# Kernel tuning notes

Measured on AMD Instinct MI355X. Metric: run time of the kernel, lower is better.

Reference implementation:

```python
import jax, jax.numpy as jnp
import numpy as np

USER, ITEM, LATDIM, HYPER, FDIM, GL, LEAKY = 100000, 200000, 64, 128, 16, 2, 0.5
N = USER + ITEM
E = 3000000
LN_EPS = 1e-5


def _leaky(x):
    return jnp.where(x > 0, x, LEAKY * x)


def _ln(x, g, b):
    m = jnp.mean(x, axis=-1, keepdims=True)
    v = jnp.mean((x - m) ** 2, axis=-1, keepdims=True)
    return (x - m) * jax.lax.rsqrt(v + LN_EPS) * g + b


def _forward(fs, rows, cols):
    (uEmbeds, iEmbeds, uHyper, iHyper, u_attn, i_attn,
     dis_W1, dis_b1, dis_W2, dis_b2, dis_Wr1, dis_br1, dis_Wr2, dis_br2,
     dis_weights, dis_ln_g, dis_ln_b,
     gate_Wg1, gate_bg1, gate_Wg2, gate_bg2, gate_Wr1, gate_br1, gate_Wr2, gate_br2,
     gate_ln_g, gate_ln_b, adj_vals) = fs
    # Attention-weighted hyperedge incidence: softmax over the node axis (dim=0)
    uu = uEmbeds @ uHyper                       # [user, hyperNum]
    uu = uu * jax.nn.softmax(uu @ u_attn, axis=0)
    ii = iEmbeds @ iHyper                       # [item, hyperNum]
    ii = ii * jax.nn.softmax(ii @ i_attn, axis=0)
    x = jnp.concatenate([uEmbeds, iEmbeds], axis=0)  # [N, latdim]
    total = x
    for i in range(GL):
        # sparse GCN: spmm(adj, x) with COO edges (keepRate == 1 -> no edge drop)
        tem = jax.ops.segment_sum(adj_vals[:, None] * x[cols], rows, num_segments=N)
        # hypergraph conv: adj @ (adj.T @ x)
        hyp = jnp.concatenate([uu @ (uu.T @ x[:USER]), ii @ (ii.T @ x[USER:])], axis=0)

        def dis(z, j):
            # 4 disentanglers, batched over k via einsum
            h = _leaky(jnp.einsum('nd,kde->kne', z, dis_W1[i, j]) + dis_b1[i, j][:, None, :])
            f = jnp.einsum('kne,kef->knf', h, dis_W2[i, j]) + dis_b2[i, j][:, None, :]  # [4,N,fdim]
            comb = jnp.einsum('k,knf->nf', jax.nn.softmax(dis_weights[i, j]), f)
            rec = _leaky(comb @ dis_Wr1[i, j] + dis_br1[i, j]) @ dis_Wr2[i, j] + dis_br2[i, j]
            return _ln(z + rec, dis_ln_g[i, j], dis_ln_b[i, j])

        def gate(cur, prev):
            c = jnp.concatenate([cur, prev], axis=-1)  # [N, 2*latdim]
            gw = jax.nn.sigmoid(jax.nn.relu(c @ gate_Wg1[i] + gate_bg1[i]) @ gate_Wg2[i] + gate_bg2[i])
            res = _leaky(c @ gate_Wr1[i] + gate_br1[i]) @ gate_Wr2[i] + gate_br2[i]
            return _ln(gw * res + cur, gate_ln_g[i], gate_ln_b[i])

        x = gate(dis(tem, 0), x) + gate(dis(hyp, 1), x)
        total = total + x
    return total  # sum(lats): final node embeddings [N, latdim]


def setup_inputs() -> dict:
    key = jax.random.key(0)
    ks = iter(jax.random.split(key, 40))

    def rn(shape, scale=0.1):
        return jax.random.normal(next(ks), shape, dtype=jnp.float32) * scale

    return dict(
        uEmbeds=rn((USER, LATDIM)),
        iEmbeds=rn((ITEM, LATDIM)),
        uHyper=rn((LATDIM, HYPER)),
        iHyper=rn((LATDIM, HYPER)),
        u_attn=rn((HYPER, 1), 1.0),
        i_attn=rn((HYPER, 1), 1.0),
        dis_W1=rn((GL, 2, 4, LATDIM, LATDIM)),
        dis_b1=jnp.zeros((GL, 2, 4, LATDIM), jnp.float32),
        dis_W2=rn((GL, 2, 4, LATDIM, FDIM)),
        dis_b2=jnp.zeros((GL, 2, 4, FDIM), jnp.float32),
        dis_Wr1=rn((GL, 2, FDIM, LATDIM)),
        dis_br1=jnp.zeros((GL, 2, LATDIM), jnp.float32),
        dis_Wr2=rn((GL, 2, LATDIM, LATDIM)),
        dis_br2=jnp.zeros((GL, 2, LATDIM), jnp.float32),
        dis_weights=jnp.ones((GL, 2, 4), jnp.float32) / 4.0,
        dis_ln_g=jnp.ones((GL, 2, LATDIM), jnp.float32),
        dis_ln_b=jnp.zeros((GL, 2, LATDIM), jnp.float32),
        gate_Wg1=rn((GL, 2 * LATDIM, LATDIM)),
        gate_bg1=jnp.zeros((GL, LATDIM), jnp.float32),
        gate_Wg2=rn((GL, LATDIM, LATDIM)),
        gate_bg2=jnp.zeros((GL, LATDIM), jnp.float32),
        gate_Wr1=rn((GL, 2 * LATDIM, LATDIM)),
        gate_br1=jnp.zeros((GL, LATDIM), jnp.float32),
        gate_Wr2=rn((GL, LATDIM, LATDIM)),
        gate_br2=jnp.zeros((GL, LATDIM), jnp.float32),
        gate_ln_g=jnp.ones((GL, LATDIM), jnp.float32),
        gate_ln_b=jnp.zeros((GL, LATDIM), jnp.float32),
        adj_vals=jax.random.uniform(next(ks), (E,), dtype=jnp.float32) * 0.1,
        adj_rows=jax.random.randint(next(ks), (E,), 0, N, dtype=jnp.int32),
        adj_cols=jax.random.randint(next(ks), (E,), 0, N, dtype=jnp.int32),
        keep_rate=1,
    )


def reference(uEmbeds, iEmbeds, uHyper, iHyper, u_attn, i_attn,
              dis_W1, dis_b1, dis_W2, dis_b2, dis_Wr1, dis_br1, dis_Wr2, dis_br2,
              dis_weights, dis_ln_g, dis_ln_b,
              gate_Wg1, gate_bg1, gate_Wg2, gate_bg2, gate_Wr1, gate_br1, gate_Wr2, gate_br2,
              gate_ln_g, gate_ln_b, adj_vals, adj_rows, adj_cols, keep_rate):
    fs = (uEmbeds, iEmbeds, uHyper, iHyper, u_attn, i_attn,
          dis_W1, dis_b1, dis_W2, dis_b2, dis_Wr1, dis_br1, dis_Wr2, dis_br2,
          dis_weights, dis_ln_g, dis_ln_b,
          gate_Wg1, gate_bg1, gate_Wg2, gate_bg2, gate_Wr1, gate_br1, gate_Wr2, gate_br2,
          gate_ln_g, gate_ln_b, adj_vals)
    return _forward(fs, adj_rows, adj_cols)
```

## Files before the change

kernel.cpp:

```cpp
#include <hip/hip_runtime.h>
#include <math.h>

#define USERN 100000
#define ITEMN 200000
#define NND   300000
#define DD    64
#define HH    128
#define FF    16
#define EDG   3000000
#define LEAKY_A 0.5f
#define LN_EPS  1e-5f
#define SCHUNK 1024
#define SNB ((NND+SCHUNK-1)/SCHUNK)
#define PROWS (NND/8)
#define VQ 81910.0f

typedef __attribute__((ext_vector_type(8))) short bf16x8;
typedef __attribute__((ext_vector_type(4))) float f32x4;
#define MFMA16(a,b,c) __builtin_amdgcn_mfma_f32_16x16x32_bf16(a,b,c,0,0,0)
#define NTL(p) __builtin_nontemporal_load(p)

__device__ __forceinline__ float leaky(float x){ return x>0.f ? x : LEAKY_A*x; }
__device__ __forceinline__ unsigned fenc(float f){ unsigned u=__float_as_uint(f); return (u&0x80000000u)? ~u : (u|0x80000000u); }
__device__ __forceinline__ float fdec(unsigned u){ return (u&0x80000000u)? __uint_as_float(u&0x7fffffffu) : __uint_as_float(~u); }
__device__ __forceinline__ short f2bf(float f){
  unsigned u=__float_as_uint(f);
  unsigned r=u + 0x7fffu + ((u>>16)&1u);
  return (short)(r>>16);
}
__device__ __forceinline__ unsigned f2bf2(float lo, float hi){
  unsigned r;
  asm("v_cvt_pk_bf16_f32 %0, %1, %2" : "=v"(r) : "v"(lo), "v"(hi));
  return r;
}
__device__ __forceinline__ float bf2f(short s){
  return __uint_as_float(((unsigned)(unsigned short)s)<<16);
}
__device__ __forceinline__ bf16x8 loadAbf(const short* __restrict__ base, int l, int dbase){
  const short* p = base + (size_t)(l&15)*DD + dbase + ((l>>4)<<2);
  int2 a=*(const int2*)p;
  int2 b=*(const int2*)(p+16);
  bf16x8 r;
  ((int2*)&r)[0]=a; ((int2*)&r)[1]=b;
  return r;
}

__global__ __launch_bounds__(256) void k_init(const float* __restrict__ uE, const float* __restrict__ iE,
                        short* __restrict__ x){
  int tot=NND*DD;
  for(int idx=blockIdx.x*256+threadIdx.x; idx<tot; idx+=gridDim.x*256){
    float v=(idx<USERN*DD)? uE[idx] : iE[idx-USERN*DD];
    x[idx]=f2bf(v);
  }
}

__global__ __launch_bounds__(128) void k_hv(const float* __restrict__ uH,const float* __restrict__ iH,
      const float* __restrict__ uA,const float* __restrict__ iA,float* __restrict__ hv){
  int t=threadIdx.x;
  const float* H=(t<64)? uH:iH;
  const float* A=(t<64)? uA:iA;
  int d=t&63;
  float s=0.f;
  for(int h=0;h<HH;h++) s=fmaf(H[d*HH+h],A[h],s);
  hv[t]=s;
}

__global__ __launch_bounds__(256) void k_att(const float* __restrict__ E, const float* __restrict__ hvp,
      float* __restrict__ a, int U){
  __shared__ float hs[64];
  int tid=threadIdx.x;
  if(tid<64) hs[tid]=hvp[tid];
  __syncthreads();
  int wave=tid>>6, lane=tid&63;
  for(int g=blockIdx.x*4+wave; g<U/4; g+=gridDim.x*4){
    int n0=g*4;
    #pragma unroll
    for(int m=0;m<4;m++){
      float p=E[(size_t)(n0+m)*DD+lane]*hs[lane];
      #pragma unroll
      for(int off=32;off;off>>=1) p+=__shfl_xor(p,off,64);
      if(lane==0) a[n0+m]=p;
    }
  }
}

__global__ __launch_bounds__(256) void k_redmax(const float* __restrict__ a, int n, unsigned* slot){
  float v=-3.0e38f;
  for(int i=blockIdx.x*256+threadIdx.x;i<n;i+=gridDim.x*256) v=fmaxf(v,a[i]);
  #pragma unroll
  for(int off=32;off;off>>=1) v=fmaxf(v,__shfl_xor(v,off,64));
  if((threadIdx.x&63)==0) atomicMax(slot, fenc(v));
}

__global__ __launch_bounds__(256) void k_sumexp(const float* __restrict__ a, int n,
      const unsigned* __restrict__ mslot, float* ssum){
  float mx=fdec(*mslot);
  float s=0.f;
  for(int i=blockIdx.x*256+threadIdx.x;i<n;i+=gridDim.x*256) s+=expf(a[i]-mx);
  #pragma unroll
  for(int off=32;off;off>>=1) s+=__shfl_xor(s,off,64);
  if((threadIdx.x&63)==0) atomicAdd(ssum, s);
}

__global__ __launch_bounds__(256) void k_scale_a(float* __restrict__ a,int n,
      const unsigned* __restrict__ mslot,const float* __restrict__ ssum){
  float mx=fdec(*mslot); float inv=1.f/(*ssum);
  for(int i=blockIdx.x*256+threadIdx.x;i<n;i+=gridDim.x*256) a[i]=expf(a[i]-mx)*inv;
}

__global__ __launch_bounds__(256) void k_hist8(const int* __restrict__ rows, int* __restrict__ cnt){
  int part=blockIdx.x&7;
  int bip=blockIdx.x>>3, nbp=gridDim.x>>3;
  int lo=part*PROWS, hi=lo+PROWS;
  for(int e=bip*256+threadIdx.x; e<EDG; e+=nbp*256){
    int r=NTL(rows+e);
    if(r>=lo && r<hi) atomicAdd(&cnt[r],1);
  }
}

__global__ __launch_bounds__(256) void k_scanA(int* __restrict__ cnt, int* __restrict__ bsum){
  __shared__ int part[256];
  int b=blockIdx.x, t=threadIdx.x;
  int base=b*SCHUNK;
  int v[4]; int s=0;
  #pragma unroll
  for(int k2=0;k2<4;k2++){
    int idx=base+t*4+k2;
    int val=(idx<NND)? cnt[idx]:0;
    v[k2]=s; s+=val;
  }
  part[t]=s;
  __syncthreads();
  for(int off=1;off<256;off<<=1){
    int y=(t>=off)? part[t-off]:0;
    __syncthreads();
    part[t]+=y;
    __syncthreads();
  }
  int excl=(t==0)?0:part[t-1];
  #pragma unroll
  for(int k2=0;k2<4;k2++){
    int idx=base+t*4+k2;
    if(idx<NND) cnt[idx]=excl+v[k2];
  }
  if(t==255) bsum[b]=part[255];
}

__global__ __launch_bounds__(512) void k_scanB(int* __restrict__ bsum){
  __shared__ int part[512];
  int t=threadIdx.x;
  part[t]=(t<SNB)? bsum[t]:0;
  __syncthreads();
  for(int off=1;off<512;off<<=1){
    int y=(t>=off)? part[t-off]:0;
    __syncthreads();
    part[t]+=y;
    __syncthreads();
  }
  if(t<SNB) bsum[t]=(t==0)?0:part[t-1];
}

__global__ __launch_bounds__(256) void k_scanC(int* __restrict__ rowptr, const int* __restrict__ bsum,
      int* __restrict__ wcur){
  for(int i=blockIdx.x*256+threadIdx.x; i<NND; i+=gridDim.x*256){
    int v=rowptr[i]+bsum[i>>10];
    rowptr[i]=v; wcur[i]=v;
  }
  if(blockIdx.x==0 && threadIdx.x==0) rowptr[NND]=EDG;
}

__global__ __launch_bounds__(256) void k_scatter8(const int* __restrict__ rows,const int* __restrict__ cols,
      const float* __restrict__ vals, int* __restrict__ wcur, unsigned* __restrict__ epack){
  int part=blockIdx.x&7;
  int bip=blockIdx.x>>3, nbp=gridDim.x>>3;
  int lo=part*PROWS, hi=lo+PROWS;
  for(int e=bip*256+threadIdx.x; e<EDG; e+=nbp*256){
    int r=NTL(rows+e);
    if(r>=lo && r<hi){
      int pos=atomicAdd(&wcur[r],1);
      unsigned q=(unsigned)(NTL(vals+e)*VQ + 0.5f);
      epack[pos]=((unsigned)NTL(cols+e)<<13) | (q & 8191u);
    }
  }
}

__global__ __launch_bounds__(512) void k_spmm_csr(const int* __restrict__ rowptr,
      const unsigned* __restrict__ epack,
      const short* __restrict__ x, short* __restrict__ tem){
  int wave=threadIdx.x>>6, q4=(threadIdx.x>>4)&3, ln=threadIdx.x&15;
  const float dq=1.0f/VQ;
  for(int r=blockIdx.x*32+wave*4+q4; r<NND; r+=gridDim.x*32){
    int st=rowptr[r], en=rowptr[r+1];
    float a0=0.f,a1=0.f,a2=0.f,a3=0.f;
    int p=st;
    for(; p+1<en; p+=2){
      unsigned w0=NTL(epack+p), w1=NTL(epack+p+1);
      int c0=w0>>13, c1=w1>>13;
      float v0=(float)(w0&8191u)*dq, v1=(float)(w1&8191u)*dq;
      int2 x0=*(const int2*)(x+(size_t)c0*DD+ln*4);
      int2 x1=*(const int2*)(x+(size_t)c1*DD+ln*4);
      a0=fmaf(v0, bf2f((short)(x0.x&0xffff)), a0);
      a1=fmaf(v0, bf2f((short)(x0.x>>16)),    a1);
      a2=fmaf(v0, bf2f((short)(x0.y&0xffff)), a2);
      a3=fmaf(v0, bf2f((short)(x0.y>>16)),    a3);
      a0=fmaf(v1, bf2f((short)(x1.x&0xffff)), a0);
      a1=fmaf(v1, bf2f((short)(x1.x>>16)),    a1);
      a2=fmaf(v1, bf2f((short)(x1.y&0xffff)), a2);
      a3=fmaf(v1, bf2f((short)(x1.y>>16)),    a3);
    }
    if(p<en){
      unsigned w0=NTL(epack+p);
      int c0=w0>>13;
      float v0=(float)(w0&8191u)*dq;
      int2 x0=*(const int2*)(x+(size_t)c0*DD+ln*4);
      a0=fmaf(v0, bf2f((short)(x0.x&0xffff)), a0);
      a1=fmaf(v0, bf2f((short)(x0.x>>16)),    a1);
      a2=fmaf(v0, bf2f((short)(x0.y&0xffff)), a2);
      a3=fmaf(v0, bf2f((short)(x0.y>>16)),    a3);
    }
    int2 outw;
    outw.x=(int)f2bf2(a0,a1);
    outw.y=(int)f2bf2(a2,a3);
    *(int2*)(tem+(size_t)r*DD+ln*4) = outw;
  }
}

__global__ __launch_bounds__(256) void k_gacc(const float* __restrict__ E,const float* __restrict__ sca,
      const short* __restrict__ x,float* __restrict__ G,int U){
  __shared__ __align__(16) float es[4][256];
  int tid=threadIdx.x, wave=tid>>6, lane=tid&63;
  float acc[64];
  #pragma unroll
  for(int j=0;j<64;j++) acc[j]=0.f;
  float* esw=es[wave];
  for(int g=blockIdx.x*4+wave; g<U/4; g+=gridDim.x*4){
    int n0=g*4;
    float xv[4];
    #pragma unroll
    for(int m=0;m<4;m++){
      float sc=sca[n0+m];
      esw[m*64+lane]=E[(size_t)(n0+m)*DD+lane]*sc;
      xv[m]=bf2f(x[(size_t)(n0+m)*DD+lane]);
    }
    #pragma unroll
    for(int d4=0;d4<16;d4++){
      float4 eb[4];
      #pragma unroll
      for(int m=0;m<4;m++) eb[m]=((const float4*)(esw+m*64))[d4];
      #pragma unroll
      for(int c=0;c<4;c++){
        #pragma unroll
        for(int m=0;m<4;m++) acc[d4*4+c]=fmaf(((const float*)&eb[m])[c],xv[m],acc[d4*4+c]);
      }
    }
  }
  #pragma unroll
  for(int j=0;j<64;j++) atomicAdd(&G[j*64+lane],acc[j]);
}

__global__ __launch_bounds__(256) void k_tm(const float* __restrict__ uH,const float* __restrict__ iH,
      const float* __restrict__ G,float* __restrict__ Mo){
  __shared__ __align__(16) float Hs[64*HH];
  __shared__ __align__(16) float Gs[64*64];
  __shared__ __align__(16) float Ts[HH*64];
  const float* H = blockIdx.x ? iH : uH;
  const float* Gp = G + blockIdx.x*4096;
  float* Mp = Mo + blockIdx.x*4096;
  int tid=threadIdx.x;
  for(int k=tid;k<64*HH;k+=256) Hs[k]=H[k];
  for(int k=tid;k<4096;k+=256) Gs[k]=Gp[k];
  __syncthreads();
  int lane=tid&63, wq=tid>>6;
  float tac[32];
  #pragma unroll
  for(int k=0;k<32;k++) tac[k]=0.f;
  for(int d1=0;d1<64;d1++){
    float gv=Gs[d1*64+lane];
    const float4* hrow=(const float4*)(Hs+d1*HH+wq*32);
    #pragma unroll
    for(int k4=0;k4<8;k4++){
      float4 hb=hrow[k4];
      tac[k4*4+0]=fmaf(hb.x,gv,tac[k4*4+0]);
      tac[k4*4+1]=fmaf(hb.y,gv,tac[k4*4+1]);
      tac[k4*4+2]=fmaf(hb.z,gv,tac[k4*4+2]);
      tac[k4*4+3]=fmaf(hb.w,gv,tac[k4*4+3]);
    }
  }
  #pragma unroll
  for(int k=0;k<32;k++) Ts[(wq*32+k)*64+lane]=tac[k];
  __syncthreads();
  float mac[16];
  #pragma unroll
  for(int k=0;k<16;k++) mac[k]=0.f;
  for(int h=0;h<HH;h++){
    float tv=Ts[h*64+lane];
    #pragma unroll
    for(int k=0;k<16;k++) mac[k]=fmaf(Hs[(wq*16+k)*HH+h],tv,mac[k]);
  }
  #pragma unroll
  for(int k=0;k<16;k++) Mp[(wq*16+k)*64+lane]=mac[k];
}

__global__ __launch_bounds__(256) void k_hyp2(const float* __restrict__ E,const float* __restrict__ sca,
      const float* __restrict__ Mp,short* __restrict__ hyp,int U){
  __shared__ __align__(16) float es[4][256];
  int tid=threadIdx.x, wave=tid>>6, lane=tid&63;
  float mcol[64];
  #pragma unroll
  for(int j=0;j<64;j++) mcol[j]=Mp[j*64+lane];
  float* esw=es[wave];
  for(int g=blockIdx.x*4+wave; g<U/4; g+=gridDim.x*4){
    int n0=g*4;
    #pragma unroll
    for(int m=0;m<4;m++){
      float sc=sca[n0+m];
      esw[m*64+lane]=E[(size_t)(n0+m)*DD+lane]*sc;
    }
    float acc[4]={0,0,0,0};
    #pragma unroll
    for(int d4=0;d4<16;d4++){
      float4 eb[4];
      #pragma unroll
      for(int m=0;m<4;m++) eb[m]=((const float4*)(esw+m*64))[d4];
      #pragma unroll
      for(int c=0;c<4;c++){
        float mv=mcol[d4*4+c];
        #pragma unroll
        for(int m=0;m<4;m++) acc[m]=fmaf(((const float*)&eb[m])[c],mv,acc[m]);
      }
    }
    unsigned p01=f2bf2(acc[0],acc[1]), p23=f2bf2(acc[2],acc[3]);
    hyp[(size_t)(n0+0)*DD+lane]=(short)p01;
    hyp[(size_t)(n0+1)*DD+lane]=(short)(p01>>16);
    hyp[(size_t)(n0+2)*DD+lane]=(short)p23;
    hyp[(size_t)(n0+3)*DD+lane]=(short)(p23>>16);
  }
}

__global__ __launch_bounds__(512) void k_dis2(
    short* __restrict__ tem, short* __restrict__ hyp,
    const float* __restrict__ W1b,const float* __restrict__ b1b,
    const float* __restrict__ W2b,const float* __restrict__ b2b,
    const float* __restrict__ Wr1b,const float* __restrict__ br1b,
    const float* __restrict__ Wr2b,const float* __restrict__ br2b,
    const float* __restrict__ wsoftb,const float* __restrict__ lngb,const float* __restrict__ lnbb,
    int layer){
  __shared__ __align__(16) short w1s[16384];
  __shared__ __align__(16) short w2s[4096];
  __shared__ __align__(16) short wr1s[2048];
  __shared__ __align__(16) short wr2s[4096];
  __shared__ __align__(16) short hst[8][1024];
  __shared__ __align__(16) short cst[8][512];
  __shared__ float swsh[4];
  int half=gridDim.x>>1;
  int sel=(blockIdx.x>=half);
  int bid=blockIdx.x - (sel? half:0);
  int ij=layer*2+sel;
  short* z = sel? hyp : tem;
  const float* W1 = W1b + (size_t)ij*4*64*64;
  const float* b1 = b1b + (size_t)ij*4*64;
  const float* W2 = W2b + (size_t)ij*4*64*16;
  const float* b2 = b2b + (size_t)ij*4*16;
  const float* Wr1= Wr1b+ (size_t)ij*16*64;
  const float* br1= br1b+ (size_t)ij*64;
  const float* Wr2= Wr2b+ (size_t)ij*64*64;
  const float* br2= br2b+ (size_t)ij*64;
  const float* wsoft=wsoftb+(size_t)ij*4;
  const float* lng= lngb + (size_t)ij*64;
  const float* lnb= lnbb + (size_t)ij*64;
  int tid=threadIdx.x;
  for(int t=tid;t<16384;t+=512){
    int j=t&7,kg=(t>>3)&3,c=(t>>5)&15,ot=(t>>9)&3,kb=(t>>11)&1,kk=t>>12;
    int k=kb*32+kg*4+(j&3)+((j>>2)<<4), o=ot*16+c;
    w1s[t]=f2bf(W1[(size_t)(kk*64+k)*64+o]);
  }
  for(int t=tid;t<4096;t+=512){
    int j=t&7,kg=(t>>3)&3,c=(t>>5)&15,kb=(t>>9)&1,kk=t>>10;
    int k=kb*32+kg*4+(j&3)+((j>>2)<<4);
    w2s[t]=f2bf(W2[(size_t)(kk*64+k)*16+c]);
  }
  for(int t=tid;t<2048;t+=512){
    int j=t&7,kg=(t>>3)&3,c=(t>>5)&15,ot=t>>9;
    int o=ot*16+c;
    short v=0;
    if(j<4){ int k=kg*4+j; v=f2bf(Wr1[k*64+o]); }
    wr1s[t]=v;
  }
  for(int t=tid;t<4096;t+=512){
    int j=t&7,kg=(t>>3)&3,c=(t>>5)&15,ot=(t>>9)&3,kb=t>>11;
    int k=kb*32+kg*4+(j&3)+((j>>2)<<4), o=ot*16+c;
    wr2s[t]=f2bf(Wr2[k*64+o]);
  }
  if(tid==0){
    float m0=fmaxf(fmaxf(wsoft[0],wsoft[1]),fmaxf(wsoft[2],wsoft[3]));
    float e0=expf(wsoft[0]-m0),e1=expf(wsoft[1]-m0),e2=expf(wsoft[2]-m0),e3=expf(wsoft[3]-m0);
    float s=e0+e1+e2+e3;
    swsh[0]=e0/s; swsh[1]=e1/s; swsh[2]=e2/s; swsh[3]=e3/s;
  }
  __syncthreads();
  int wave=tid>>6, l=tid&63, lr=l&15, lg=l>>4;
  float sw[4]; sw[0]=swsh[0]; sw[1]=swsh[1]; sw[2]=swsh[2]; sw[3]=swsh[3];
  float b1v[4][4], br1v[4], br2v[4], gv[4], bv[4];
  #pragma unroll
  for(int kk=0;kk<4;kk++)
    #pragma unroll
    for(int ot=0;ot<4;ot++) b1v[kk][ot]=b1[kk*64+ot*16+lr];
  float b2c = sw[0]*b2[lr] + sw[1]*b2[16+lr] + sw[2]*b2[32+lr] + sw[3]*b2[48+lr];
  #pragma unroll
  for(int ot=0;ot<4;ot++){
    br1v[ot]=br1[ot*16+lr]; br2v[ot]=br2[ot*16+lr];
    gv[ot]=lng[ot*16+lr];   bv[ot]=lnb[ot*16+lr];
  }
  short* hw=hst[wave];
  short* cw=cst[wave];
  for(int t=l;t<256;t+=64){
    int r=t>>4, lgp=(t>>2)&3, jj=t&3;
    cw[(r*4+lgp)*8+4+jj]=0;
  }
  int slot=(lr*4+lg)*8;
  int sbase=((lg*4)*4 + (lr>>2))*8 + (l&3);
  const f32x4 zero={0.f,0.f,0.f,0.f};
  for(int tile=bid*8+wave; tile<NND/16; tile+=half*8){
    int n0=tile*16;
    short* zrow=z+(size_t)n0*DD;
    bf16x8 A0=loadAbf(zrow,l,0), A1=loadAbf(zrow,l,32);
    f32x4 cba; cba[0]=b2c; cba[1]=b2c; cba[2]=b2c; cba[3]=b2c;
    #pragma unroll
    for(int kk=0;kk<4;kk++){
      const short* w1k=&w1s[kk*4096];
      #pragma unroll
      for(int ot=0;ot<4;ot++){
        f32x4 ha=zero;
        ha=MFMA16(A0,*(const bf16x8*)&w1k[ot*512+slot],ha);
        ha=MFMA16(A1,*(const bf16x8*)&w1k[2048+ot*512+slot],ha);
        float bb=b1v[kk][ot];
        unsigned p01=f2bf2(leaky(ha[0]+bb), leaky(ha[1]+bb));
        unsigned p23=f2bf2(leaky(ha[2]+bb), leaky(ha[3]+bb));
        int base=(ot>>1)*512 + sbase + ((ot&1)<<2);
        hw[base   ]=(short)p01;
        hw[base+32]=(short)(p01>>16);
        hw[base+64]=(short)p23;
        hw[base+96]=(short)(p23>>16);
      }
      bf16x8 hA0=*(const bf16x8*)&hw[slot];
      bf16x8 hA1=*(const bf16x8*)&hw[512+slot];
      f32x4 fa=zero;
      fa=MFMA16(hA0,*(const bf16x8*)&w2s[kk*1024+slot],fa);
      fa=MFMA16(hA1,*(const bf16x8*)&w2s[kk*1024+512+slot],fa);
      float swk=sw[kk];
      #pragma unroll
      for(int j=0;j<4;j++) cba[j]=fmaf(swk,fa[j],cba[j]);
    }
    {
      int cbase=((lg*4)*4 + (lr>>2))*8 + (lr&3);
      unsigned c01=f2bf2(cba[0],cba[1]), c23=f2bf2(cba[2],cba[3]);
      cw[cbase   ]=(short)c01;
      cw[cbase+32]=(short)(c01>>16);
      cw[cbase+64]=(short)c23;
      cw[cbase+96]=(short)(c23>>16);
    }
    bf16x8 cA=*(const bf16x8*)&cw[slot];
    #pragma unroll
    for(int ot=0;ot<4;ot++){
      f32x4 ra=MFMA16(cA,*(const bf16x8*)&wr1s[ot*512+slot],zero);
      float bb=br1v[ot];
      unsigned p01=f2bf2(leaky(ra[0]+bb), leaky(ra[1]+bb));
      unsigned p23=f2bf2(leaky(ra[2]+bb), leaky(ra[3]+bb));
      int base=(ot>>1)*512 + sbase + ((ot&1)<<2);
      hw[base   ]=(short)p01;
      hw[base+32]=(short)(p01>>16);
      hw[base+64]=(short)p23;
      hw[base+96]=(short)(p23>>16);
    }
    bf16x8 rA0=*(const bf16x8*)&hw[slot];
    bf16x8 rA1=*(const bf16x8*)&hw[512+slot];
    float y[4][4];
    #pragma unroll
    for(int ot=0;ot<4;ot++){
      f32x4 rc=zero;
      rc=MFMA16(rA0,*(const bf16x8*)&wr2s[ot*512+slot],rc);
      rc=MFMA16(rA1,*(const bf16x8*)&wr2s[2048+ot*512+slot],rc);
      #pragma unroll
      for(int j=0;j<4;j++){
        float zd=bf2f(zrow[(size_t)(lg*4+j)*DD + ot*16+lr]);
        y[ot][j]=zd + rc[j] + br2v[ot];
      }
    }
    #pragma unroll
    for(int j=0;j<4;j++){
      float s=y[0][j]+y[1][j]+y[2][j]+y[3][j];
      s+=__shfl_xor(s,1,64); s+=__shfl_xor(s,2,64); s+=__shfl_xor(s,4,64); s+=__shfl_xor(s,8,64);
      float mean=s*(1.f/64.f);
      float t0=y[0][j]-mean, t1=y[1][j]-mean, t2=y[2][j]-mean, t3=y[3][j]-mean;
      float s2=t0*t0+t1*t1+t2*t2+t3*t3;
      s2+=__shfl_xor(s2,1,64); s2+=__shfl_xor(s2,2,64); s2+=__shfl_xor(s2,4,64); s2+=__shfl_xor(s2,8,64);
      float inv=rsqrtf(s2*(1.f/64.f)+LN_EPS);
      unsigned q01=f2bf2(t0*inv*gv[0]+bv[0], t1*inv*gv[1]+bv[1]);
      unsigned q23=f2bf2(t2*inv*gv[2]+bv[2], t3*inv*gv[3]+bv[3]);
      size_t row=(size_t)(lg*4+j)*DD;
      zrow[row +  0+lr]=(short)q01;
      zrow[row + 16+lr]=(short)(q01>>16);
      zrow[row + 32+lr]=(short)q23;
      zrow[row + 48+lr]=(short)(q23>>16);
    }
  }
}

__global__ __launch_bounds__(512) void k_gate2(
    const short* __restrict__ tem, const short* __restrict__ hyp,
    const short* __restrict__ xin, short* __restrict__ xout,
    const float* __restrict__ uEo, const float* __restrict__ iEo, float* __restrict__ outp, int doOut,
    const float* __restrict__ Wg1,const float* __restrict__ bg1,
    const float* __restrict__ Wg2,const float* __restrict__ bg2,
    const float* __restrict__ Wr1,const float* __restrict__ br1,
    const float* __restrict__ Wr2,const float* __restrict__ br2,
    const float* __restrict__ lng,const float* __restrict__ lnb){
  __shared__ __align__(16) short g1s[4*4*512];
  __shared__ __align__(16) short r1s[4*4*512];
  __shared__ __align__(16) short g2s[2*4*512];
  __shared__ __align__(16) short r2s[2*4*512];
  __shared__ __align__(16) short hls[8][2][1024];
  int tid=threadIdx.x;
  for(int t=tid;t<8192;t+=512){
    int j=t&7,kg=(t>>3)&3,c=(t>>5)&15,ot=(t>>9)&3,kb=t>>11;
    int k=kb*32+kg*4+(j&3)+((j>>2)<<4), o=ot*16+c;
    g1s[t]=f2bf(Wg1[k*64+o]);
    r1s[t]=f2bf(Wr1[k*64+o]);
  }
  for(int t=tid;t<4096;t+=512){
    int j=t&7,kg=(t>>3)&3,c=(t>>5)&15,ot=(t>>9)&3,kb=t>>11;
    int k=kb*32+kg*4+(j&3)+((j>>2)<<4), o=ot*16+c;
    g2s[t]=f2bf(Wg2[k*64+o]);
    r2s[t]=f2bf(Wr2[k*64+o]);
  }
  __syncthreads();
  int wave=tid>>6, l=tid&63;
  int lr=l&15, lg=l>>4;
  float bg1v[4],br1v[4],bg2v[4],br2v[4],gv[4],bv[4];
  #pragma unroll
  for(int ot=0;ot<4;ot++){
    bg1v[ot]=bg1[ot*16+lr]; br1v[ot]=br1[ot*16+lr];
    bg2v[ot]=bg2[ot*16+lr]; br2v[ot]=br2[ot*16+lr];
    gv[ot]=lng[ot*16+lr];   bv[ot]=lnb[ot*16+lr];
  }
  short* hG=&hls[wave][0][0];
  short* hR=&hls[wave][1][0];
  int slot=(lr*4+lg)*8;
  int sbase=((lg*4)*4 + (lr>>2))*8 + (l&3);
  const f32x4 zero={0.f,0.f,0.f,0.f};
  for(int tile=blockIdx.x*8+wave; tile<NND/16; tile+=gridDim.x*8){
    int n0=tile*16;
    const short* xrow=xin+(size_t)n0*DD;
    bf16x8 pA0=loadAbf(xrow,l,0), pA1=loadAbf(xrow,l,32);
    f32x4 pg[4],pr[4];
    #pragma unroll
    for(int ot=0;ot<4;ot++){
      f32x4 ag=zero, ar=zero;
      ag=MFMA16(pA0,*(const bf16x8*)&g1s[(2*4+ot)*512+slot],ag);
      ag=MFMA16(pA1,*(const bf16x8*)&g1s[(3*4+ot)*512+slot],ag);
      ar=MFMA16(pA0,*(const bf16x8*)&r1s[(2*4+ot)*512+slot],ar);
      ar=MFMA16(pA1,*(const bf16x8*)&r1s[(3*4+ot)*512+slot],ar);
      pg[ot]=ag; pr[ot]=ar;
    }
    float ya[4][4];
    #pragma unroll
    for(int p=0;p<2;p++){
      const short* cur=(p? hyp : tem)+(size_t)n0*DD;
      bf16x8 cA0=loadAbf(cur,l,0), cA1=loadAbf(cur,l,32);
      #pragma unroll
      for(int ot=0;ot<4;ot++){
        f32x4 ag=pg[ot], ar=pr[ot];
        ag=MFMA16(cA0,*(const bf16x8*)&g1s[(0*4+ot)*512+slot],ag);
        ag=MFMA16(cA1,*(const bf16x8*)&g1s[(1*4+ot)*512+slot],ag);
        ar=MFMA16(cA0,*(const bf16x8*)&r1s[(0*4+ot)*512+slot],ar);
        ar=MFMA16(cA1,*(const bf16x8*)&r1s[(1*4+ot)*512+slot],ar);
        float bgv=bg1v[ot], brv=br1v[ot];
        unsigned g01=f2bf2(fmaxf(ag[0]+bgv,0.f), fmaxf(ag[1]+bgv,0.f));
        unsigned g23=f2bf2(fmaxf(ag[2]+bgv,0.f), fmaxf(ag[3]+bgv,0.f));
        unsigned r01=f2bf2(leaky(ar[0]+brv), leaky(ar[1]+brv));
        unsigned r23=f2bf2(leaky(ar[2]+brv), leaky(ar[3]+brv));
        int base=(ot>>1)*512 + sbase + ((ot&1)<<2);
        hG[base   ]=(short)g01;  hG[base+32]=(short)(g01>>16);
        hG[base+64]=(short)g23;  hG[base+96]=(short)(g23>>16);
        hR[base   ]=(short)r01;  hR[base+32]=(short)(r01>>16);
        hR[base+64]=(short)r23;  hR[base+96]=(short)(r23>>16);
      }
      bf16x8 hgA0=*(const bf16x8*)&hG[slot],    hgA1=*(const bf16x8*)&hG[512+slot];
      bf16x8 hrA0=*(const bf16x8*)&hR[slot],    hrA1=*(const bf16x8*)&hR[512+slot];
      f32x4 g2a[4], r2a[4];
      #pragma unroll
      for(int ot=0;ot<4;ot++){
        f32x4 ag=zero, ar=zero;
        ag=MFMA16(hgA0,*(const bf16x8*)&g2s[(0*4+ot)*512+slot],ag);
        ag=MFMA16(hgA1,*(const bf16x8*)&g2s[(1*4+ot)*512+slot],ag);
        ar=MFMA16(hrA0,*(const bf16x8*)&r2s[(0*4+ot)*512+slot],ar);
        ar=MFMA16(hrA1,*(const bf16x8*)&r2s[(1*4+ot)*512+slot],ar);
        g2a[ot]=ag; r2a[ot]=ar;
      }
      float y[4][4];
      #pragma unroll
      for(int ot=0;ot<4;ot++){
        #pragma unroll
        for(int j=0;j<4;j++){
          float cd=bf2f(cur[(size_t)(lg*4+j)*DD + ot*16+lr]);
          float gw=1.f/(1.f+expf(-(g2a[ot][j]+bg2v[ot])));
          y[ot][j]=gw*(r2a[ot][j]+br2v[ot])+cd;
        }
      }
      #pragma unroll
      for(int j=0;j<4;j++){
        float s=y[0][j]+y[1][j]+y[2][j]+y[3][j];
        s+=__shfl_xor(s,1,64); s+=__shfl_xor(s,2,64); s+=__shfl_xor(s,4,64); s+=__shfl_xor(s,8,64);
        float mean=s*(1.f/64.f);
        float t0=y[0][j]-mean, t1=y[1][j]-mean, t2=y[2][j]-mean, t3=y[3][j]-mean;
        float s2=t0*t0+t1*t1+t2*t2+t3*t3;
        s2+=__shfl_xor(s2,1,64); s2+=__shfl_xor(s2,2,64); s2+=__shfl_xor(s2,4,64); s2+=__shfl_xor(s2,8,64);
        float inv=rsqrtf(s2*(1.f/64.f)+LN_EPS);
        float yn0=t0*inv*gv[0]+bv[0];
        float yn1=t1*inv*gv[1]+bv[1];
        float yn2=t2*inv*gv[2]+bv[2];
        float yn3=t3*inv*gv[3]+bv[3];
        if(p==0){ ya[0][j]=yn0; ya[1][j]=yn1; ya[2][j]=yn2; ya[3][j]=yn3; }
        else    { ya[0][j]+=yn0; ya[1][j]+=yn1; ya[2][j]+=yn2; ya[3][j]+=yn3; }
      }
    }
    if(doOut){
      const float* embr = (n0<USERN)? (uEo + (size_t)n0*DD) : (iEo + (size_t)(n0-USERN)*DD);
      #pragma unroll
      for(int j=0;j<4;j++){
        size_t rowi=(size_t)(n0+lg*4+j)*DD + lr;
        size_t loc=(size_t)(lg*4+j)*DD + lr;
        unsigned o01=f2bf2(ya[0][j],ya[1][j]), o23=f2bf2(ya[2][j],ya[3][j]);
        xout[rowi   ]=(short)o01;  xout[rowi+16]=(short)(o01>>16);
        xout[rowi+32]=(short)o23;  xout[rowi+48]=(short)(o23>>16);
        outp[rowi   ]=embr[loc   ] + bf2f(xin[rowi   ]) + ya[0][j];
        outp[rowi+16]=embr[loc+16] + bf2f(xin[rowi+16]) + ya[1][j];
        outp[rowi+32]=embr[loc+32] + bf2f(xin[rowi+32]) + ya[2][j];
        outp[rowi+48]=embr[loc+48] + bf2f(xin[rowi+48]) + ya[3][j];
      }
    }else{
      #pragma unroll
      for(int j=0;j<4;j++){
        size_t rowi=(size_t)(n0+lg*4+j)*DD + lr;
        unsigned o01=f2bf2(ya[0][j],ya[1][j]), o23=f2bf2(ya[2][j],ya[3][j]);
        xout[rowi   ]=(short)o01;  xout[rowi+16]=(short)(o01>>16);
        xout[rowi+32]=(short)o23;  xout[rowi+48]=(short)(o23>>16);
      }
    }
  }
}

extern "C" void kernel_launch(void* const* d_in, const int* in_sizes, int n_in,
                              void* d_out, int out_size, void* d_ws, size_t ws_size,
                              hipStream_t stream){
  const float* uE  =(const float*)d_in[0];
  const float* iE  =(const float*)d_in[1];
  const float* uH  =(const float*)d_in[2];
  const float* iH  =(const float*)d_in[3];
  const float* uA  =(const float*)d_in[4];
  const float* iA  =(const float*)d_in[5];
  const float* dW1 =(const float*)d_in[6];
  const float* db1 =(const float*)d_in[7];
  const float* dW2 =(const float*)d_in[8];
  const float* db2 =(const float*)d_in[9];
  const float* dWr1=(const float*)d_in[10];
  const float* dbr1=(const float*)d_in[11];
  const float* dWr2=(const float*)d_in[12];
  const float* dbr2=(const float*)d_in[13];
  const float* dwts=(const float*)d_in[14];
  const float* dlng=(const float*)d_in[15];
  const float* dlnb=(const float*)d_in[16];
  const float* gWg1=(const float*)d_in[17];
  const float* gbg1=(const float*)d_in[18];
  const float* gWg2=(const float*)d_in[19];
  const float* gbg2=(const float*)d_in[20];
  const float* gWr1=(const float*)d_in[21];
  const float* gbr1=(const float*)d_in[22];
  const float* gWr2=(const float*)d_in[23];
  const float* gbr2=(const float*)d_in[24];
  const float* glng=(const float*)d_in[25];
  const float* glnb=(const float*)d_in[26];
  const float* avals=(const float*)d_in[27];
  const int*   arows=(const int*)d_in[28];
  const int*   acols=(const int*)d_in[29];
  float* out=(float*)d_out;

  size_t bfShorts = (size_t)4*NND*DD;
  size_t f32Floats = (size_t)NND + 128 + 8192 + 8192 + 8;
  size_t csrFloats = (size_t)EDG + (NND+1) + NND + 512;
  size_t needBase = bfShorts*sizeof(short) + f32Floats*sizeof(float);
  size_t needFull = needBase + csrFloats*sizeof(float);
  if(ws_size < needBase) return;
  bool persist = (ws_size >= needFull);

  short* xA  = (short*)d_ws;
  short* xB  = xA  + (size_t)NND*DD;
  short* tem = xB  + (size_t)NND*DD;
  short* hyp = tem + (size_t)NND*DD;
  float* a   = (float*)(hyp + (size_t)NND*DD);
  float* hv  = a   + NND;
  float* G   = hv  + 128;
  float* Mb  = G   + 8192;
  float* red = Mb  + 8192;

  float* csrbase = persist ? (red + 8) : (float*)hyp;
  unsigned* epack = (unsigned*)csrbase;
  int*   rowptr= (int*)(csrbase + (size_t)EDG);
  int*   wcur  = rowptr + (NND+1);
  int*   bsum  = wcur + NND;

  hipMemsetAsync(red, 0, 8*sizeof(float), stream);
  k_init<<<2048,256,0,stream>>>(uE,iE,xA);
  k_hv<<<1,128,0,stream>>>(uH,iH,uA,iA,hv);
  k_att<<<256,256,0,stream>>>(uE,hv,a,USERN);
  k_att<<<256,256,0,stream>>>(iE,hv+64,a+USERN,ITEMN);
  k_redmax<<<256,256,0,stream>>>(a,USERN,(unsigned*)red);
  k_redmax<<<256,256,0,stream>>>(a+USERN,ITEMN,(unsigned*)red+2);
  k_sumexp<<<256,256,0,stream>>>(a,USERN,(const unsigned*)red,red+1);
  k_sumexp<<<256,256,0,stream>>>(a+USERN,ITEMN,(const unsigned*)red+2,red+3);
  k_scale_a<<<256,256,0,stream>>>(a,USERN,(const unsigned*)red,red+1);
  k_scale_a<<<256,256,0,stream>>>(a+USERN,ITEMN,(const unsigned*)red+2,red+3);

  if(persist){
    hipMemsetAsync(rowptr,0,(NND+1)*sizeof(int),stream);
    k_hist8<<<2048,256,0,stream>>>(arows,rowptr);
    k_scanA<<<SNB,256,0,stream>>>(rowptr,bsum);
    k_scanB<<<1,512,0,stream>>>(bsum);
    k_scanC<<<2048,256,0,stream>>>(rowptr,bsum,wcur);
    k_scatter8<<<2048,256,0,stream>>>(arows,acols,avals,wcur,epack);
  }

  for(int i=0;i<2;i++){
    short* xin = (i==0)? xA : xB;
    short* xout= (i==0)? xB : xA;
    if(!persist){
      hipMemsetAsync(rowptr,0,(NND+1)*sizeof(int),stream);
      k_hist8<<<2048,256,0,stream>>>(arows,rowptr);
      k_scanA<<<SNB,256,0,stream>>>(rowptr,bsum);
      k_scanB<<<1,512,0,stream>>>(bsum);
      k_scanC<<<2048,256,0,stream>>>(rowptr,bsum,wcur);
      k_scatter8<<<2048,256,0,stream>>>(arows,acols,avals,wcur,epack);
    }
    k_spmm_csr<<<4096,512,0,stream>>>(rowptr,epack,xin,tem);

    hipMemsetAsync(G,0,8192*sizeof(float),stream);
    k_gacc<<<256,256,0,stream>>>(uE,a,xin,G,USERN);
    k_gacc<<<256,256,0,stream>>>(iE,a+USERN,xin+(size_t)USERN*DD,G+4096,ITEMN);
    k_tm<<<2,256,0,stream>>>(uH,iH,G,Mb);
    k_hyp2<<<256,256,0,stream>>>(uE,a,Mb,hyp,USERN);
    k_hyp2<<<256,256,0,stream>>>(iE,a+USERN,Mb+4096,hyp+(size_t)USERN*DD,ITEMN);
    k_dis2<<<1024,512,0,stream>>>(tem,hyp,
      dW1,db1,dW2,db2,dWr1,dbr1,dWr2,dbr2,dwts,dlng,dlnb,i);
    k_gate2<<<512,512,0,stream>>>(tem,hyp,xin,xout,
      uE,iE,out,(i==1)?1:0,
      gWg1+(size_t)i*128*64, gbg1+(size_t)i*64,
      gWg2+(size_t)i*64*64,  gbg2+(size_t)i*64,
      gWr1+(size_t)i*128*64, gbr1+(size_t)i*64,
      gWr2+(size_t)i*64*64,  gbr2+(size_t)i*64,
      glng+(size_t)i*64, glnb+(size_t)i*64);
  }
}
```

Baseline: 1.736 ms.

## Pre-swizzle bf16 weights once and read MFMA B operands from global memory

Adds a one-time kernel that converts and swizzles the gate and disentangler weights to bf16 in the workspace. k_dis2 and k_gate2 drop their per-block shared-memory weight staging and barrier, and read B fragments directly from global (L1/L2-cached) memory. This removes redundant per-block conversion work and cuts LDS use, which may raise occupancy. In exchange, the inner MFMA loops now issue global loads instead of LDS reads, which may carry higher latency.

Result: slower. 1.947 ms (+12.1%).

```diff
diff --git a/kernel.cpp b/kernel.cpp
--- a/kernel.cpp
+++ b/kernel.cpp
@@ -14,6 +14,8 @@
 #define SNB ((NND+SCHUNK-1)/SCHUNK)
 #define PROWS (NND/8)
 #define VQ 81910.0f
+#define GWSZ 24576
+#define DWSZ 26624
 
 typedef __attribute__((ext_vector_type(8))) short bf16x8;
 typedef __attribute__((ext_vector_type(4))) float f32x4;
@@ -43,6 +45,66 @@
   bf16x8 r;
   ((int2*)&r)[0]=a; ((int2*)&r)[1]=b;
   return r;
+}
+__device__ __forceinline__ bf16x8 loadB(const short* __restrict__ p){
+  int4 v=*(const int4*)p;
+  bf16x8 r; *(int4*)&r=v; return r;
+}
+
+__global__ __launch_bounds__(256) void k_prepw(
+    const float* __restrict__ gWg1,const float* __restrict__ gWr1,
+    const float* __restrict__ gWg2,const float* __restrict__ gWr2,
+    const float* __restrict__ dW1,const float* __restrict__ dW2,
+    const float* __restrict__ dWr1,const float* __restrict__ dWr2,
+    short* __restrict__ gw, short* __restrict__ dw){
+  int tot=2*GWSZ + 4*DWSZ;
+  for(int idx=blockIdx.x*256+threadIdx.x; idx<tot; idx+=gridDim.x*256){
+    if(idx < 2*GWSZ){
+      int li=idx/GWSZ, t2=idx%GWSZ;
+      short v;
+      if(t2<16384){
+        int t=t2&8191;
+        int j=t&7,kg=(t>>3)&3,c=(t>>5)&15,ot=(t>>9)&3,kb=t>>11;
+        int k=kb*32+kg*4+(j&3)+((j>>2)<<4), o=ot*16+c;
+        const float* W=(t2<8192)? gWg1 : gWr1;
+        v=f2bf(W[(size_t)li*8192 + k*64+o]);
+      }else{
+        int t=(t2-16384)&4095;
+        int j=t&7,kg=(t>>3)&3,c=(t>>5)&15,ot=(t>>9)&3,kb=t>>11;
+        int k=kb*32+kg*4+(j&3)+((j>>2)<<4), o=ot*16+c;
+        const float* W=(t2<20480)? gWg2 : gWr2;
+        v=f2bf(W[(size_t)li*4096 + k*64+o]);
+      }
+      gw[idx]=v;
+    }else{
+      int d=idx-2*GWSZ;
+      int ij=d/DWSZ, t2=d%DWSZ;
+      short v;
+      if(t2<16384){
+        int t=t2;
+        int j=t&7,kg=(t>>3)&3,c=(t>>5)&15,ot=(t>>9)&3,kb=(t>>11)&1,kk=t>>12;
+        int k=kb*32+kg*4+(j&3)+((j>>2)<<4), o=ot*16+c;
+        v=f2bf(dW1[(size_t)ij*16384 + (size_t)(kk*64+k)*64+o]);
+      }else if(t2<20480){
+        int t=t2-16384;
+        int j=t&7,kg=(t>>3)&3,c=(t>>5)&15,kb=(t>>9)&1,kk=t>>10;
+        int k=kb*32+kg*4+(j&3)+((j>>2)<<4);
+        v=f2bf(dW2[(size_t)ij*4096 + (size_t)(kk*64+k)*16+c]);
+      }else if(t2<22528){
+        int t=t2-20480;
+        int j=t&7,kg=(t>>3)&3,c=(t>>5)&15,ot=t>>9;
+        int o=ot*16+c;
+        v=0;
+        if(j<4){ int k=kg*4+j; v=f2bf(dWr1[(size_t)ij*1024 + k*64+o]); }
+      }else{
+        int t=t2-22528;
+        int j=t&7,kg=(t>>3)&3,c=(t>>5)&15,ot=(t>>9)&3,kb=t>>11;
+        int k=kb*32+kg*4+(j&3)+((j>>2)<<4), o=ot*16+c;
+        v=f2bf(dWr2[(size_t)ij*4096 + k*64+o]);
+      }
+      dw[d]=v;
+    }
+  }
 }
 
 __global__ __launch_bounds__(256) void k_init(const float* __restrict__ uE, const float* __restrict__ iE,
@@ -339,67 +401,39 @@
 
 __global__ __launch_bounds__(512) void k_dis2(
     short* __restrict__ tem, short* __restrict__ hyp,
-    const float* __restrict__ W1b,const float* __restrict__ b1b,
-    const float* __restrict__ W2b,const float* __restrict__ b2b,
-    const float* __restrict__ Wr1b,const float* __restrict__ br1b,
-    const float* __restrict__ Wr2b,const float* __restrict__ br2b,
+    const short* __restrict__ dw,
+    const float* __restrict__ b1b,const float* __restrict__ b2b,
+    const float* __restrict__ br1b,const float* __restrict__ br2b,
     const float* __restrict__ wsoftb,const float* __restrict__ lngb,const float* __restrict__ lnbb,
     int layer){
-  __shared__ __align__(16) short w1s[16384];
-  __shared__ __align__(16) short w2s[4096];
-  __shared__ __align__(16) short wr1s[2048];
-  __shared__ __align__(16) short wr2s[4096];
   __shared__ __align__(16) short hst[8][1024];
   __shared__ __align__(16) short cst[8][512];
-  __shared__ float swsh[4];
   int half=gridDim.x>>1;
   int sel=(blockIdx.x>=half);
   int bid=blockIdx.x - (sel? half:0);
   int ij=layer*2+sel;
   short* z = sel? hyp : tem;
-  const float* W1 = W1b + (size_t)ij*4*64*64;
+  const short* w1s = dw + (size_t)ij*DWSZ;
+  const short* w2s = w1s + 16384;
+  const short* wr1s= w1s + 20480;
+  const short* wr2s= w1s + 22528;
   const float* b1 = b1b + (size_t)ij*4*64;
-  const float* W2 = W2b + (size_t)ij*4*64*16;
   const float* b2 = b2b + (size_t)ij*4*16;
-  const float* Wr1= Wr1b+ (size_t)ij*16*64;
   const float* br1= br1b+ (size_t)ij*64;
-  const float* Wr2= Wr2b+ (size_t)ij*64*64;
   const float* br2= br2b+ (size_t)ij*64;
   const float* wsoft=wsoftb+(size_t)ij*4;
   const float* lng= lngb + (size_t)ij*64;
   const float* lnb= lnbb + (size_t)ij*64;
   int tid=threadIdx.x;
-  for(int t=tid;t<16384;t+=512){
-    int j=t&7,kg=(t>>3)&3,c=(t>>5)&15,ot=(t>>9)&3,kb=(t>>11)&1,kk=t>>12;
-    int k=kb*32+kg*4+(j&3)+((j>>2)<<4), o=ot*16+c;
-    w1s[t]=f2bf(W1[(size_t)(kk*64+k)*64+o]);
-  }
-  for(int t=tid;t<4096;t+=512){
-    int j=t&7,kg=(t>>3)&3,c=(t>>5)&15,kb=(t>>9)&1,kk=t>>10;
-    int k=kb*32+kg*4+(j&3)+((j>>2)<<4);
-    w2s[t]=f2bf(W2[(size_t)(kk*64+k)*16+c]);
-  }
-  for(int t=tid;t<2048;t+=512){
-    int j=t&7,kg=(t>>3)&3,c=(t>>5)&15,ot=t>>9;
-    int o=ot*16+c;
-    short v=0;
-    if(j<4){ int k=kg*4+j; v=f2bf(Wr1[k*64+o]); }
-    wr1s[t]=v;
-  }
-  for(int t=tid;t<4096;t+=512){
-    int j=t&7,kg=(t>>3)&3,c=(t>>5)&15,ot=(t>>9)&3,kb=t>>11;
-    int k=kb*32+kg*4+(j&3)+((j>>2)<<4), o=ot*16+c;
-    wr2s[t]=f2bf(Wr2[k*64+o]);
-  }
-  if(tid==0){
-    float m0=fmaxf(fmaxf(wsoft[0],wsoft[1]),fmaxf(wsoft[2],wsoft[3]));
-    float e0=expf(wsoft[0]-m0),e1=expf(wsoft[1]-m0),e2=expf(wsoft[2]-m0),e3=expf(wsoft[3]-m0);
+  int wave=tid>>6, l=tid&63, lr=l&15, lg=l>>4;
+  float sw[4];
+  {
+    float w0=wsoft[0],w1=wsoft[1],w2=wsoft[2],w3=wsoft[3];
+    float m0=fmaxf(fmaxf(w0,w1),fmaxf(w2,w3));
+    float e0=expf(w0-m0),e1=expf(w1-m0),e2=expf(w2-m0),e3=expf(w3-m0);
     float s=e0+e1+e2+e3;
-    swsh[0]=e0/s; swsh[1]=e1/s; swsh[2]=e2/s; swsh[3]=e3/s;
-  }
-  __syncthreads();
-  int wave=tid>>6, l=tid&63, lr=l&15, lg=l>>4;
-  float sw[4]; sw[0]=swsh[0]; sw[1]=swsh[1]; sw[2]=swsh[2]; sw[3]=swsh[3];
+    sw[0]=e0/s; sw[1]=e1/s; sw[2]=e2/s; sw[3]=e3/s;
+  }
   float b1v[4][4], br1v[4], br2v[4], gv[4], bv[4];
   #pragma unroll
   for(int kk=0;kk<4;kk++)
@@ -431,8 +465,8 @@
       #pragma unroll
       for(int ot=0;ot<4;ot++){
         f32x4 ha=zero;
-        ha=MFMA16(A0,*(const bf16x8*)&w1k[ot*512+slot],ha);
-        ha=MFMA16(A1,*(const bf16x8*)&w1k[2048+ot*512+slot],ha);
+        ha=MFMA16(A0,loadB(&w1k[ot*512+slot]),ha);
+        ha=MFMA16(A1,loadB(&w1k[2048+ot*512+slot]),ha);
         float bb=b1v[kk][ot];
         unsigned p01=f2bf2(leaky(ha[0]+bb), leaky(ha[1]+bb));
         unsigned p23=f2bf2(leaky(ha[2]+bb), leaky(ha[3]+bb));
@@ -445,8 +479,8 @@
       bf16x8 hA0=*(const bf16x8*)&hw[slot];
       bf16x8 hA1=*(const bf16x8*)&hw[512+slot];
       f32x4 fa=zero;
-      fa=MFMA16(hA0,*(const bf16x8*)&w2s[kk*1024+slot],fa);
-      fa=MFMA16(hA1,*(const bf16x8*)&w2s[kk*1024+512+slot],fa);
+      fa=MFMA16(hA0,loadB(&w2s[kk*1024+slot]),fa);
+      fa=MFMA16(hA1,loadB(&w2s[kk*1024+512+slot]),fa);
       float swk=sw[kk];
       #pragma unroll
       for(int j=0;j<4;j++) cba[j]=fmaf(swk,fa[j],cba[j]);
@@ -462,7 +496,7 @@
     bf16x8 cA=*(const bf16x8*)&cw[slot];
     #pragma unroll
     for(int ot=0;ot<4;ot++){
-      f32x4 ra=MFMA16(cA,*(const bf16x8*)&wr1s[ot*512+slot],zero);
+      f32x4 ra=MFMA16(cA,loadB(&wr1s[ot*512+slot]),zero);
       float bb=br1v[ot];
       unsigned p01=f2bf2(leaky(ra[0]+bb), leaky(ra[1]+bb));
       unsigned p23=f2bf2(leaky(ra[2]+bb), leaky(ra[3]+bb));
@@ -478,8 +512,8 @@
     #pragma unroll
     for(int ot=0;ot<4;ot++){
       f32x4 rc=zero;
-      rc=MFMA16(rA0,*(const bf16x8*)&wr2s[ot*512+slot],rc);
-      rc=MFMA16(rA1,*(const bf16x8*)&wr2s[2048+ot*512+slot],rc);
+      rc=MFMA16(rA0,loadB(&wr2s[ot*512+slot]),rc);
+      rc=MFMA16(rA1,loadB(&wr2s[2048+ot*512+slot]),rc);
       #pragma unroll
       for(int j=0;j<4;j++){
         float zd=bf2f(zrow[(size_t)(lg*4+j)*DD + ot*16+lr]);
@@ -510,30 +544,16 @@
     const short* __restrict__ tem, const short* __restrict__ hyp,
     const short* __restrict__ xin, short* __restrict__ xout,
     const float* __restrict__ uEo, const float* __restrict__ iEo, float* __restrict__ outp, int doOut,
-    const float* __restrict__ Wg1,const float* __restrict__ bg1,
-    const float* __restrict__ Wg2,const float* __restrict__ bg2,
-    const float* __restrict__ Wr1,const float* __restrict__ br1,
-    const float* __restrict__ Wr2,const float* __restrict__ br2,
+    const short* __restrict__ gwl,
+    const float* __restrict__ bg1,const float* __restrict__ bg2,
+    const float* __restrict__ br1,const float* __restrict__ br2,
     const float* __restrict__ lng,const float* __restrict__ lnb){
-  __shared__ __align__(16) short g1s[4*4*512];
-  __shared__ __align__(16) short r1s[4*4*512];
-  __shared__ __align__(16) short g2s[2*4*512];
-  __shared__ __align__(16) short r2s[2*4*512];
   __shared__ __align__(16) short hls[8][2][1024];
+  const short* g1s = gwl;
+  const short* r1s = gwl + 8192;
+  const short* g2s = gwl + 16384;
+  const short* r2s = gwl + 20480;
   int tid=threadIdx.x;
-  for(int t=tid;t<8192;t+=512){
-    int j=t&7,kg=(t>>3)&3,c=(t>>5)&15,ot=(t>>9)&3,kb=t>>11;
-    int k=kb*32+kg*4+(j&3)+((j>>2)<<4), o=ot*16+c;
-    g1s[t]=f2bf(Wg1[k*64+o]);
-    r1s[t]=f2bf(Wr1[k*64+o]);
-  }
-  for(int t=tid;t<4096;t+=512){
-    int j=t&7,kg=(t>>3)&3,c=(t>>5)&15,ot=(t>>9)&3,kb=t>>11;
-    int k=kb*32+kg*4+(j&3)+((j>>2)<<4), o=ot*16+c;
-    g2s[t]=f2bf(Wg2[k*64+o]);
-    r2s[t]=f2bf(Wr2[k*64+o]);
-  }
-  __syncthreads();
   int wave=tid>>6, l=tid&63;
   int lr=l&15, lg=l>>4;
   float bg1v[4],br1v[4],bg2v[4],br2v[4],gv[4],bv[4];
@@ -556,10 +576,10 @@
     #pragma unroll
     for(int ot=0;ot<4;ot++){
       f32x4 ag=zero, ar=zero;
-      ag=MFMA16(pA0,*(const bf16x8*)&g1s[(2*4+ot)*512+slot],ag);
-      ag=MFMA16(pA1,*(const bf16x8*)&g1s[(3*4+ot)*512+slot],ag);
-      ar=MFMA16(pA0,*(const bf16x8*)&r1s[(2*4+ot)*512+slot],ar);
-      ar=MFMA16(pA1,*(const bf16x8*)&r1s[(3*4+ot)*512+slot],ar);
+      ag=MFMA16(pA0,loadB(&g1s[(2*4+ot)*512+slot]),ag);
+      ag=MFMA16(pA1,loadB(&g1s[(3*4+ot)*512+slot]),ag);
+      ar=MFMA16(pA0,loadB(&r1s[(2*4+ot)*512+slot]),ar);
+      ar=MFMA16(pA1,loadB(&r1s[(3*4+ot)*512+slot]),ar);
       pg[ot]=ag; pr[ot]=ar;
     }
     float ya[4][4];
@@ -570,10 +590,10 @@
       #pragma unroll
       for(int ot=0;ot<4;ot++){
         f32x4 ag=pg[ot], ar=pr[ot];
-        ag=MFMA16(cA0,*(const bf16x8*)&g1s[(0*4+ot)*512+slot],ag);
-        ag=MFMA16(cA1,*(const bf16x8*)&g1s[(1*4+ot)*512+slot],ag);
-        ar=MFMA16(cA0,*(const bf16x8*)&r1s[(0*4+ot)*512+slot],ar);
-        ar=MFMA16(cA1,*(const bf16x8*)&r1s[(1*4+ot)*512+slot],ar);
+        ag=MFMA16(cA0,loadB(&g1s[(0*4+ot)*512+slot]),ag);
+        ag=MFMA16(cA1,loadB(&g1s[(1*4+ot)*512+slot]),ag);
+        ar=MFMA16(cA0,loadB(&r1s[(0*4+ot)*512+slot]),ar);
+        ar=MFMA16(cA1,loadB(&r1s[(1*4+ot)*512+slot]),ar);
         float bgv=bg1v[ot], brv=br1v[ot];
         unsigned g01=f2bf2(fmaxf(ag[0]+bgv,0.f), fmaxf(ag[1]+bgv,0.f));
         unsigned g23=f2bf2(fmaxf(ag[2]+bgv,0.f), fmaxf(ag[3]+bgv,0.f));
@@ -591,10 +611,10 @@
       #pragma unroll
       for(int ot=0;ot<4;ot++){
         f32x4 ag=zero, ar=zero;
-        ag=MFMA16(hgA0,*(const bf16x8*)&g2s[(0*4+ot)*512+slot],ag);
-        ag=MFMA16(hgA1,*(const bf16x8*)&g2s[(1*4+ot)*512+slot],ag);
-        ar=MFMA16(hrA0,*(const bf16x8*)&r2s[(0*4+ot)*512+slot],ar);
-        ar=MFMA16(hrA1,*(const bf16x8*)&r2s[(1*4+ot)*512+slot],ar);
+        ag=MFMA16(hgA0,loadB(&g2s[(0*4+ot)*512+slot]),ag);
+        ag=MFMA16(hgA1,loadB(&g2s[(1*4+ot)*512+slot]),ag);
+        ar=MFMA16(hrA0,loadB(&r2s[(0*4+ot)*512+slot]),ar);
+        ar=MFMA16(hrA1,loadB(&r2s[(1*4+ot)*512+slot]),ar);
         g2a[ot]=ag; r2a[ot]=ar;
       }
       float y[4][4];
@@ -687,8 +707,9 @@
 
   size_t bfShorts = (size_t)4*NND*DD;
   size_t f32Floats = (size_t)NND + 128 + 8192 + 8192 + 8;
+  size_t wShorts = (size_t)2*GWSZ + 4*DWSZ;
   size_t csrFloats = (size_t)EDG + (NND+1) + NND + 512;
-  size_t needBase = bfShorts*sizeof(short) + f32Floats*sizeof(float);
+  size_t needBase = bfShorts*sizeof(short) + f32Floats*sizeof(float) + wShorts*sizeof(short);
   size_t needFull = needBase + csrFloats*sizeof(float);
   if(ws_size < needBase) return;
   bool persist = (ws_size >= needFull);
@@ -702,8 +723,10 @@
   float* G   = hv  + 128;
   float* Mb  = G   + 8192;
   float* red = Mb  + 8192;
-
-  float* csrbase = persist ? (red + 8) : (float*)hyp;
+  short* gw  = (short*)(red + 8);
+  short* dw  = gw + 2*GWSZ;
+
+  float* csrbase = persist ? (float*)(dw + 4*DWSZ) : (float*)hyp;
   unsigned* epack = (unsigned*)csrbase;
   int*   rowptr= (int*)(csrbase + (size_t)EDG);
   int*   wcur  = rowptr + (NND+1);
@@ -711,6 +734,7 @@
 
   hipMemsetAsync(red, 0, 8*sizeof(float), stream);
   k_init<<<2048,256,0,stream>>>(uE,iE,xA);
+  k_prepw<<<256,256,0,stream>>>(gWg1,gWr1,gWg2,gWr2,dW1,dW2,dWr1,dWr2,gw,dw);
   k_hv<<<1,128,0,stream>>>(uH,iH,uA,iA,hv);
   k_att<<<256,256,0,stream>>>(uE,hv,a,USERN);
   k_att<<<256,256,0,stream>>>(iE,hv+64,a+USERN,ITEMN);
@@ -749,14 +773,13 @@
     k_tm<<<2,256,0,stream>>>(uH,iH,G,Mb);
     k_hyp2<<<256,256,0,stream>>>(uE,a,Mb,hyp,USERN);
     k_hyp2<<<256,256,0,stream>>>(iE,a+USERN,Mb+4096,hyp+(size_t)USERN*DD,ITEMN);
-    k_dis2<<<1024,512,0,stream>>>(tem,hyp,
-      dW1,db1,dW2,db2,dWr1,dbr1,dWr2,dbr2,dwts,dlng,dlnb,i);
+    k_dis2<<<1024,512,0,stream>>>(tem,hyp,dw,
+      db1,db2,dbr1,dbr2,dwts,dlng,dlnb,i);
     k_gate2<<<512,512,0,stream>>>(tem,hyp,xin,xout,
       uE,iE,out,(i==1)?1:0,
-      gWg1+(size_t)i*128*64, gbg1+(size_t)i*64,
-      gWg2+(size_t)i*64*64,  gbg2+(size_t)i*64,
-      gWr1+(size_t)i*128*64, gbr1+(size_t)i*64,
-      gWr2+(size_t)i*64*64,  gbr2+(size_t)i*64,
+      gw+(size_t)i*GWSZ,
+      gbg1+(size_t)i*64, gbg2+(size_t)i*64,
+      gbr1+(size_t)i*64, gbr2+(size_t)i*64,
       glng+(size_t)i*64, glnb+(size_t)i*64);
   }
 }
```
